# Performance work log

Hardware: AMD Instinct MI355X
Metric: run time of the kernel (lower is better)

Reference implementation:

```python
import jax, jax.numpy as jnp
from jax import lax
import numpy as np

BN_EPS = 1e-5

def nearest_resize(x, out_h, out_w):
    # torch F.interpolate(mode='nearest'): src = floor(dst * in / out)
    B, C, H, W = x.shape
    hi = (jnp.arange(out_h) * H) // out_h
    wi = (jnp.arange(out_w) * W) // out_w
    return x[:, :, hi][:, :, :, wi]

def conv1x1(x, w, b=None):
    y = jnp.einsum('bchw,oc->bohw', x, w)
    if b is not None:
        y = y + b[None, :, None, None]
    return y

def dwconv(x, w, stride, pad):
    C = x.shape[1]
    return lax.conv_general_dilated(x, w, (stride, stride), [(pad, pad), (pad, pad)],
                                    dimension_numbers=('NCHW', 'OIHW', 'NCHW'),
                                    feature_group_count=C)

def bn(x, g, b, m, v):
    scale = g / jnp.sqrt(v + BN_EPS)
    return (x - m[None, :, None, None]) * scale[None, :, None, None] + b[None, :, None, None]


def setup_inputs() -> dict:
    key = jax.random.key(0)
    ks = jax.random.split(key, 8)
    B, C, H0, W0 = 4, 512, 192, 192
    w_scale = 0.05
    return {
        'x': jax.random.normal(ks[0], (B, C, H0, W0), jnp.float32),
        'q_w': jax.random.normal(ks[1], (C, C), jnp.float32) * w_scale,
        'q_b': jnp.zeros((C,), jnp.float32),
        'kv_w': jax.random.normal(ks[2], (2 * C, C), jnp.float32) * w_scale,
        'kv_b': jnp.zeros((2 * C,), jnp.float32),
        'sr1_w': jax.random.normal(ks[3], (C, 1, 2, 2), jnp.float32) * w_scale,
        'bn1_g': jnp.ones((C,), jnp.float32),
        'bn1_b': jnp.zeros((C,), jnp.float32),
        'bn1_m': jnp.zeros((C,), jnp.float32),
        'bn1_v': jnp.ones((C,), jnp.float32),
        'sr2_w': jax.random.normal(ks[4], (C, C), jnp.float32) * w_scale,
        'bn2_g': jnp.ones((C,), jnp.float32),
        'bn2_b': jnp.zeros((C,), jnp.float32),
        'bn2_m': jnp.zeros((C,), jnp.float32),
        'bn2_v': jnp.ones((C,), jnp.float32),
        'lc_w': jax.random.normal(ks[5], (C, 1, 3, 3), jnp.float32) * w_scale,
        'lc_b': jnp.zeros((C,), jnp.float32),
        'head_num': 8,
    }


def reference(x, q_w, q_b, kv_w, kv_b, sr1_w, bn1_g, bn1_b, bn1_m, bn1_v,
              sr2_w, bn2_g, bn2_b, bn2_m, bn2_v, lc_w, lc_b, head_num):
    origin_h, origin_w = x.shape[2], x.shape[3]
    x = nearest_resize(x, origin_h // 4, origin_w // 4)
    B, C, H, W = x.shape
    hd = C // head_num
    scale = hd ** (-0.5)

    # q projection (1x1 conv with bias)
    q = conv1x1(x, q_w, q_b)  # [B,C,H,W]

    # spatial reduction: depthwise conv(k=sr, s=sr, p=sr//2) + BN + ReLU, then 1x1 + BN
    sr = sr1_w.shape[-1]
    kv = jax.nn.relu(bn(dwconv(x, sr1_w, sr, sr // 2), bn1_g, bn1_b, bn1_m, bn1_v))
    kv = bn(conv1x1(kv, sr2_w), bn2_g, bn2_b, bn2_m, bn2_v)

    # local depthwise 3x3 conv residual
    kv = dwconv(kv, lc_w, 1, 1) + lc_b[None, :, None, None] + kv

    # kv projection (1x1 conv, 2C output)
    kv = conv1x1(kv, kv_w, kv_b)
    k, v = jnp.split(kv, 2, axis=1)  # each [B,C,Hs,Ws]
    M = k.shape[2] * k.shape[3]

    q_ = jnp.swapaxes(q.reshape(B, head_num, hd, H * W), -1, -2)  # [B,h,N,hd]
    k_ = k.reshape(B, head_num, hd, M)                             # [B,h,hd,M]
    v_ = jnp.swapaxes(v.reshape(B, head_num, hd, M), -1, -2)       # [B,h,M,hd]

    attn = jax.nn.softmax(jnp.matmul(q_, k_) * scale, axis=-1)     # [B,h,N,M]
    out = jnp.swapaxes(jnp.matmul(attn, v_), -1, -2).reshape(B, C, H, W)

    # NOTE: original torch code passes size=(origin_w, origin_h)
    out = nearest_resize(out, origin_w, origin_h)
    return out
```

## Files before the change

kernel.cpp:

```cpp
#include <hip/hip_runtime.h>

#define Bsz 4
#define Cc  512
#define C2  1024
#define H0c 192
#define Hh  48
#define Nn  2304
#define HNh 8
#define HD  64
#define Hs  25
#define Ms  625

typedef const float* fp;
typedef _Float16 f16;
typedef __attribute__((ext_vector_type(8))) _Float16 f16x8;
typedef __attribute__((ext_vector_type(4))) _Float16 f16x4;
typedef __attribute__((ext_vector_type(4))) float    f32x4;

__global__ __launch_bounds__(256) void k_downsample(fp __restrict__ x,
                                                    float* __restrict__ xds) {
    int idx = blockIdx.x * 256 + threadIdx.x;
    if (idx >= Bsz * Cc * Nn) return;
    int j  = idx % Hh;
    int i  = (idx / Hh) % Hh;
    int bc = idx / Nn;
    xds[idx] = x[((size_t)bc * H0c + i * 4) * H0c + j * 4];
}

__global__ __launch_bounds__(256) void k_transpose(const float* __restrict__ in,
                                                   f16* __restrict__ out,
                                                   int R, int S,
                                                   size_t in_bs, size_t out_bs) {
    __shared__ float tile[32][33];
    const float* inb = in + (size_t)blockIdx.z * in_bs;
    f16* outb = out + (size_t)blockIdx.z * out_bs;
    int s0 = blockIdx.x * 32, r0 = blockIdx.y * 32;
    int t = threadIdx.x;
    #pragma unroll
    for (int p = 0; p < 4; p++) {
        int e = t + p * 256; int i = e >> 5, j = e & 31;
        float v = 0.f;
        if (r0 + i < R && s0 + j < S) v = inb[(size_t)(r0 + i) * S + s0 + j];
        tile[i][j] = v;
    }
    __syncthreads();
    #pragma unroll
    for (int p = 0; p < 4; p++) {
        int e = t + p * 256; int oi = e >> 5, oj = e & 31;
        if (s0 + oi < S && r0 + oj < R)
            outb[(size_t)(s0 + oi) * R + r0 + oj] = (f16)tile[oj][oi];
    }
}

__global__ __launch_bounds__(256) void k_gemm_mfma(
    const float* __restrict__ W, const f16* __restrict__ Xt,
    float* __restrict__ Yf, f16* __restrict__ Yt,
    const int Md, const int Nd, const int NtRows, const int mode,
    fp __restrict__ bias,
    fp __restrict__ bn_g, fp __restrict__ bn_b, fp __restrict__ bn_m, fp __restrict__ bn_v)
{
    __shared__ f16 sA[128 * 80];
    __shared__ f16 sB[128 * 80];
    const int b  = blockIdx.z;
    const int m0 = blockIdx.y * 128, n0 = blockIdx.x * 128;
    const int t = threadIdx.x;
    const int lane = t & 63, w = t >> 6;
    const int lm = lane & 15, q = lane >> 4;
    const int wm = w >> 1, wn = w & 1;
    const f16* Xb = Xt + (size_t)b * Nd * 512;

    f32x4 acc[4][4];
    #pragma unroll
    for (int i = 0; i < 4; i++)
        #pragma unroll
        for (int j = 0; j < 4; j++)
            #pragma unroll
            for (int r = 0; r < 4; r++) acc[i][j][r] = 0.f;

    for (int k0 = 0; k0 < 512; k0 += 64) {
        {
            int r = t >> 1, hh = (t & 1) * 32;
            const float* wr = W + (size_t)(m0 + r) * 512 + k0 + hh;
            f16* dst = &sA[r * 80 + hh];
            #pragma unroll
            for (int i = 0; i < 8; i++) {
                float4 v = *(const float4*)&wr[i * 4];
                f16x4 h4; h4[0] = (f16)v.x; h4[1] = (f16)v.y; h4[2] = (f16)v.z; h4[3] = (f16)v.w;
                *(f16x4*)&dst[i * 4] = h4;
            }
        }
        {
            int r = t >> 1, hh = (t & 1) * 32;
            bool ok = (n0 + r) < Nd;
            const f16* xr = Xb + (size_t)(n0 + r) * 512 + k0 + hh;
            f16* dst = &sB[r * 80 + hh];
            #pragma unroll
            for (int i = 0; i < 4; i++) {
                f16x8 v;
                if (ok) {
                    v = *(const f16x8*)&xr[i * 8];
                } else {
                    for (int z = 0; z < 8; z++) v[z] = (f16)0.f;
                }
                *(f16x8*)&dst[i * 8] = v;
            }
        }
        __syncthreads();
        #pragma unroll
        for (int ks = 0; ks < 2; ks++) {
            f16x8 af[4], bf[4];
            #pragma unroll
            for (int i = 0; i < 4; i++)
                af[i] = *(const f16x8*)&sA[(wm * 64 + i * 16 + lm) * 80 + ks * 32 + q * 8];
            #pragma unroll
            for (int j = 0; j < 4; j++)
                bf[j] = *(const f16x8*)&sB[(wn * 64 + j * 16 + lm) * 80 + ks * 32 + q * 8];
            #pragma unroll
            for (int i = 0; i < 4; i++)
                #pragma unroll
                for (int j = 0; j < 4; j++)
                    acc[i][j] = __builtin_amdgcn_mfma_f32_16x16x32_f16(af[i], bf[j], acc[i][j], 0, 0, 0);
        }
        __syncthreads();
    }

    #pragma unroll
    for (int i = 0; i < 4; i++) {
        int ob = m0 + wm * 64 + i * 16 + q * 4;
        float badd[4], bsc[4], bsh[4];
        #pragma unroll
        for (int r = 0; r < 4; r++) {
            int o = ob + r;
            badd[r] = bias ? bias[o] : 0.f;
            if (bn_g) { bsc[r] = bn_g[o] * rsqrtf(bn_v[o] + 1e-5f); bsh[r] = bn_b[o] - bn_m[o] * bsc[r]; }
            else      { bsc[r] = 1.f; bsh[r] = 0.f; }
        }
        #pragma unroll
        for (int j = 0; j < 4; j++) {
            int n = n0 + wn * 64 + j * 16 + lm;
            if (n >= Nd) continue;
            f32x4 a = acc[i][j];
            if (mode == 0) {
                #pragma unroll
                for (int r = 0; r < 4; r++)
                    Yf[((size_t)b * Md + ob + r) * Nd + n] = (a[r] + badd[r]) * bsc[r] + bsh[r];
            } else if (mode == 1 || (mode == 2 && ob < 512)) {
                f16x4 h;
                #pragma unroll
                for (int r = 0; r < 4; r++) h[r] = (f16)(a[r] + badd[r]);
                int hh = ob >> 6, d0 = ob & 63;
                *(f16x4*)&Yt[((size_t)(b * 8 + hh) * NtRows + n) * 64 + d0] = h;
            } else {
                #pragma unroll
                for (int r = 0; r < 4; r++)
                    Yf[((size_t)b * 512 + (ob + r - 512)) * Nd + n] = a[r] + badd[r];
            }
        }
    }
}

__global__ __launch_bounds__(256) void k_sr1(const float* __restrict__ xds, fp __restrict__ w,
                                             fp g, fp bb, fp bm, fp bv,
                                             float* __restrict__ kv1) {
    int idx = blockIdx.x * 256 + threadIdx.x;
    if (idx >= Bsz * Cc * Ms) return;
    int wo = idx % Hs, ho = (idx / Hs) % Hs, bc = idx / Ms;
    int c = bc % Cc;
    const float* src = xds + (size_t)bc * Nn;
    float acc = 0.f;
    #pragma unroll
    for (int di = 0; di < 2; di++) {
        int ih = ho * 2 - 1 + di;
        if (ih < 0 || ih >= Hh) continue;
        #pragma unroll
        for (int dj = 0; dj < 2; dj++) {
            int iw = wo * 2 - 1 + dj;
            if (iw < 0 || iw >= Hh) continue;
            acc += w[c * 4 + di * 2 + dj] * src[ih * Hh + iw];
        }
    }
    float sc = g[c] * rsqrtf(bv[c] + 1e-5f);
    float y = (acc - bm[c]) * sc + bb[c];
    kv1[idx] = fmaxf(y, 0.f);
}

__global__ __launch_bounds__(256) void k_lc(const float* __restrict__ kv2, fp __restrict__ w,
                                            fp __restrict__ lb, float* __restrict__ kv3) {
    int idx = blockIdx.x * 256 + threadIdx.x;
    if (idx >= Bsz * Cc * Ms) return;
    int wo = idx % Hs, ho = (idx / Hs) % Hs, bc = idx / Ms;
    int c = bc % Cc;
    const float* src = kv2 + (size_t)bc * Ms;
    float acc = 0.f;
    #pragma unroll
    for (int di = 0; di < 3; di++) {
        int ih = ho - 1 + di;
        if (ih < 0 || ih >= Hs) continue;
        #pragma unroll
        for (int dj = 0; dj < 3; dj++) {
            int iw = wo - 1 + dj;
            if (iw < 0 || iw >= Hs) continue;
            acc += w[c * 9 + di * 3 + dj] * src[ih * Hs + iw];
        }
    }
    kv3[idx] = acc + lb[c] + src[ho * Hs + wo];
}

__global__ __launch_bounds__(256) void k_cvtv(const float* __restrict__ vbuf,
                                              f16* __restrict__ vt) {
    int idx = blockIdx.x * 256 + threadIdx.x;
    if (idx >= Bsz * Cc * 640) return;
    int col = idx % 640, row = idx / 640;
    vt[idx] = (f16)((col < Ms) ? vbuf[(size_t)row * Ms + col] : 0.f);
}

__global__ __launch_bounds__(256) void k_attn_mfma(
    const f16* __restrict__ Qt, const f16* __restrict__ Kt,
    const f16* __restrict__ Vt, float* __restrict__ Obuf)
{
    __shared__ f16 sK[64 * 80];
    __shared__ f16 sV[64 * 80];
    __shared__ f16 sP[4][16 * 80];

    int bh = blockIdx.y;
    int n0 = blockIdx.x * 64;
    int t = threadIdx.x, w = t >> 6, lane = t & 63;
    int lm = lane & 15, q = lane >> 4;
    f16* sPw = &sP[w][0];

    f16x8 qf[2];
    {
        const f16* qrow = Qt + ((size_t)bh * Nn + n0 + w * 16 + lm) * 64;
        qf[0] = *(const f16x8*)&qrow[q * 8];
        qf[1] = *(const f16x8*)&qrow[32 + q * 8];
    }

    f32x4 od[4];
    #pragma unroll
    for (int dt = 0; dt < 4; dt++)
        #pragma unroll
        for (int r = 0; r < 4; r++) od[dt][r] = 0.f;
    float mold[4], lold[4];
    #pragma unroll
    for (int r = 0; r < 4; r++) { mold[r] = -1e30f; lold[r] = 0.f; }

    int kr = t >> 2, kc = t & 3;
    const f16* kbase = Kt + (size_t)bh * 640 * 64;
    const f16* vbase = Vt + (size_t)bh * 64 * 640;

    for (int mc = 0; mc < 640; mc += 64) {
        {
            const f16* ksrc = kbase + (size_t)(mc + kr) * 64;
            *(f16x8*)&sK[kr * 80 + kc * 8]      = *(const f16x8*)&ksrc[kc * 8];
            *(f16x8*)&sK[kr * 80 + 32 + kc * 8] = *(const f16x8*)&ksrc[32 + kc * 8];
            const f16* vsrc = vbase + (size_t)kr * 640 + mc;
            *(f16x8*)&sV[kr * 80 + kc * 8]      = *(const f16x8*)&vsrc[kc * 8];
            *(f16x8*)&sV[kr * 80 + 32 + kc * 8] = *(const f16x8*)&vsrc[32 + kc * 8];
        }
        __syncthreads();

        f32x4 sc4[4];
        #pragma unroll
        for (int j = 0; j < 4; j++)
            #pragma unroll
            for (int r = 0; r < 4; r++) sc4[j][r] = 0.f;
        #pragma unroll
        for (int ks = 0; ks < 2; ks++) {
            #pragma unroll
            for (int j = 0; j < 4; j++) {
                f16x8 kf = *(const f16x8*)&sK[(j * 16 + lm) * 80 + ks * 32 + q * 8];
                sc4[j] = __builtin_amdgcn_mfma_f32_16x16x32_f16(qf[ks], kf, sc4[j], 0, 0, 0);
            }
        }

        #pragma unroll
        for (int reg = 0; reg < 4; reg++) {
            float mx = -1e30f;
            #pragma unroll
            for (int j = 0; j < 4; j++) {
                float s = sc4[j][reg] * 0.125f;
                if (mc + j * 16 + lm >= Ms) s = -1e30f;
                sc4[j][reg] = s;
                mx = fmaxf(mx, s);
            }
            #pragma unroll
            for (int off = 1; off < 16; off <<= 1) mx = fmaxf(mx, __shfl_xor(mx, off));
            float mnew = fmaxf(mold[reg], mx);
            float alpha = __expf(mold[reg] - mnew);
            float rs = 0.f;
            #pragma unroll
            for (int j = 0; j < 4; j++) {
                float p = __expf(sc4[j][reg] - mnew);
                sc4[j][reg] = p;
                rs += p;
            }
            #pragma unroll
            for (int off = 1; off < 16; off <<= 1) rs += __shfl_xor(rs, off);
            lold[reg] = lold[reg] * alpha + rs;
            mold[reg] = mnew;
            #pragma unroll
            for (int dt = 0; dt < 4; dt++) od[dt][reg] *= alpha;
            #pragma unroll
            for (int j = 0; j < 4; j++)
                sPw[(q * 4 + reg) * 80 + j * 16 + lm] = (f16)sc4[j][reg];
        }

        #pragma unroll
        for (int ks = 0; ks < 2; ks++) {
            f16x8 pa = *(const f16x8*)&sPw[lm * 80 + ks * 32 + q * 8];
            #pragma unroll
            for (int dt = 0; dt < 4; dt++) {
                f16x8 vf = *(const f16x8*)&sV[(dt * 16 + lm) * 80 + ks * 32 + q * 8];
                od[dt] = __builtin_amdgcn_mfma_f32_16x16x32_f16(pa, vf, od[dt], 0, 0, 0);
            }
        }
        __syncthreads();
    }

    float inv[4];
    #pragma unroll
    for (int r = 0; r < 4; r++) inv[r] = 1.f / lold[r];
    #pragma unroll
    for (int dt = 0; dt < 4; dt++) {
        f32x4 o;
        #pragma unroll
        for (int r = 0; r < 4; r++) o[r] = od[dt][r] * inv[r];
        size_t c = (size_t)bh * 64 + dt * 16 + lm;
        *(f32x4*)&Obuf[c * Nn + n0 + w * 16 + q * 4] = o;
    }
}

__global__ __launch_bounds__(256) void k_upsample(const float* __restrict__ O,
                                                  float* __restrict__ out) {
    size_t idx = (size_t)blockIdx.x * 256 + threadIdx.x;
    if (idx >= (size_t)Bsz * Cc * H0c * 48) return;
    int jg = (int)(idx % 48);
    int i  = (int)((idx / 48) % H0c);
    int bc = (int)(idx / ((size_t)48 * H0c));
    float s = O[(size_t)bc * Nn + (i >> 2) * Hh + jg];
    float4 pack = make_float4(s, s, s, s);
    *(float4*)(out + ((size_t)bc * H0c + i) * H0c + jg * 4) = pack;
}

extern "C" void kernel_launch(void* const* d_in, const int* in_sizes, int n_in,
                              void* d_out, int out_size, void* d_ws, size_t ws_size,
                              hipStream_t stream) {
    (void)in_sizes; (void)n_in; (void)out_size; (void)ws_size;
    fp x     = (fp)d_in[0];
    fp q_w   = (fp)d_in[1];
    fp q_b   = (fp)d_in[2];
    fp kv_w  = (fp)d_in[3];
    fp kv_b  = (fp)d_in[4];
    fp sr1_w = (fp)d_in[5];
    fp bn1_g = (fp)d_in[6];
    fp bn1_b = (fp)d_in[7];
    fp bn1_m = (fp)d_in[8];
    fp bn1_v = (fp)d_in[9];
    fp sr2_w = (fp)d_in[10];
    fp bn2_g = (fp)d_in[11];
    fp bn2_b = (fp)d_in[12];
    fp bn2_m = (fp)d_in[13];
    fp bn2_v = (fp)d_in[14];
    fp lc_w  = (fp)d_in[15];
    fp lc_b  = (fp)d_in[16];
    float* out = (float*)d_out;

    float* ws   = (float*)d_ws;
    float* A    = ws;
    float* xds  = A;
    float* Obuf = A;
    float* kv3  = A + 3400000;
    float* Bv   = A + 4718592;
    f16*   xt   = (f16*)Bv;
    float* kv2  = Bv;
    float* Cq   = Bv + 2359296;
    f16*   Qt   = (f16*)Cq;
    float* Dv   = Cq + 2359296;
    float* kv1  = Dv;
    float* vbuf = Dv;
    float* Ev   = Dv + 1280000;
    f16*   kv1t = (f16*)Ev;
    f16*   kv3t = (f16*)Ev;
    float* Fv   = Ev + 640000;
    f16*   Kt   = (f16*)Fv;
    float* Gv   = Fv + 655360;
    f16*   vt   = (f16*)Gv;

    k_downsample<<<Bsz * Cc * Nn / 256, 256, 0, stream>>>(x, xds);
    k_transpose<<<dim3(72, 16, Bsz), 256, 0, stream>>>(xds, xt, Cc, Nn,
                                                       (size_t)Cc * Nn, (size_t)Nn * Cc);
    k_gemm_mfma<<<dim3(18, 4, Bsz), 256, 0, stream>>>(q_w, xt, nullptr, Qt,
        Cc, Nn, Nn, 1, q_b, nullptr, nullptr, nullptr, nullptr);
    k_sr1<<<Bsz * Cc * Ms / 256, 256, 0, stream>>>(xds, sr1_w, bn1_g, bn1_b, bn1_m, bn1_v, kv1);
    k_transpose<<<dim3(20, 16, Bsz), 256, 0, stream>>>(kv1, kv1t, Cc, Ms,
                                                       (size_t)Cc * Ms, (size_t)Ms * Cc);
    k_gemm_mfma<<<dim3(5, 4, Bsz), 256, 0, stream>>>(sr2_w, kv1t, kv2, nullptr,
        Cc, Ms, 0, 0, nullptr, bn2_g, bn2_b, bn2_m, bn2_v);
    k_lc<<<Bsz * Cc * Ms / 256, 256, 0, stream>>>(kv2, lc_w, lc_b, kv3);
    k_transpose<<<dim3(20, 16, Bsz), 256, 0, stream>>>(kv3, kv3t, Cc, Ms,
                                                       (size_t)Cc * Ms, (size_t)Ms * Cc);
    k_gemm_mfma<<<dim3(5, 8, Bsz), 256, 0, stream>>>(kv_w, kv3t, vbuf, Kt,
        C2, Ms, 640, 2, kv_b, nullptr, nullptr, nullptr, nullptr);
    k_cvtv<<<Bsz * Cc * 640 / 256, 256, 0, stream>>>(vbuf, vt);
    k_attn_mfma<<<dim3(Nn / 64, Bsz * HNh), 256, 0, stream>>>(Qt, Kt, vt, Obuf);
    k_upsample<<<(unsigned)((size_t)Bsz * Cc * H0c * 48 / 256), 256, 0, stream>>>(Obuf, out);
}
```

Baseline: 651.5 us.

## Fuse elementwise stages into neighbouring kernels and write upsampled output from attention

Merges the downsample with the transpose, the spatial-reduction depthwise conv and the local 3x3 conv with their transposes, and the V fp16 conversion into the kv GEMM epilogue. The attention kernel now writes the 4x4 nearest-upsampled output directly, which removes the Obuf round trip and the separate upsample launch. This cuts several kernel launches and intermediate fp32 buffers, and the workspace layout is reorganised to match. The attention epilogue's scattered float4 stores across rows may be less coalesced than the old dedicated upsample kernel.

```diff
diff --git a/kernel.cpp b/kernel.cpp
--- a/kernel.cpp
+++ b/kernel.cpp
@@ -17,44 +17,115 @@
 typedef __attribute__((ext_vector_type(4))) _Float16 f16x4;
 typedef __attribute__((ext_vector_type(4))) float    f32x4;
 
-__global__ __launch_bounds__(256) void k_downsample(fp __restrict__ x,
-                                                    float* __restrict__ xds) {
-    int idx = blockIdx.x * 256 + threadIdx.x;
-    if (idx >= Bsz * Cc * Nn) return;
-    int j  = idx % Hh;
-    int i  = (idx / Hh) % Hh;
-    int bc = idx / Nn;
-    xds[idx] = x[((size_t)bc * H0c + i * 4) * H0c + j * 4];
-}
-
-__global__ __launch_bounds__(256) void k_transpose(const float* __restrict__ in,
-                                                   f16* __restrict__ out,
-                                                   int R, int S,
-                                                   size_t in_bs, size_t out_bs) {
+__global__ __launch_bounds__(256) void k_ds_t(fp __restrict__ x,
+                                              float* __restrict__ xds,
+                                              f16* __restrict__ xt) {
     __shared__ float tile[32][33];
-    const float* inb = in + (size_t)blockIdx.z * in_bs;
-    f16* outb = out + (size_t)blockIdx.z * out_bs;
-    int s0 = blockIdx.x * 32, r0 = blockIdx.y * 32;
-    int t = threadIdx.x;
+    const int b = blockIdx.z;
+    const int s0 = blockIdx.x * 32, r0 = blockIdx.y * 32;
+    const int t = threadIdx.x;
+    const float* xb = x + (size_t)b * Cc * H0c * H0c;
+    float* xdsb = xds + (size_t)b * Cc * Nn;
     #pragma unroll
     for (int p = 0; p < 4; p++) {
         int e = t + p * 256; int i = e >> 5, j = e & 31;
+        int c = r0 + i, n = s0 + j;
+        float v = xb[((size_t)c * H0c + (n / Hh) * 4) * H0c + (n % Hh) * 4];
+        tile[i][j] = v;
+        xdsb[(size_t)c * Nn + n] = v;
+    }
+    __syncthreads();
+    #pragma unroll
+    for (int p = 0; p < 4; p++) {
+        int e = t + p * 256; int oi = e >> 5, oj = e & 31;
+        xt[((size_t)b * Nn + s0 + oi) * Cc + r0 + oj] = (f16)tile[oj][oi];
+    }
+}
+
+__global__ __launch_bounds__(256) void k_sr1t(const float* __restrict__ xds,
+                                              fp __restrict__ w, fp g, fp bb, fp bm, fp bv,
+                                              f16* __restrict__ kv1t) {
+    __shared__ float tile[32][33];
+    const int b = blockIdx.z;
+    const int s0 = blockIdx.x * 32, r0 = blockIdx.y * 32;
+    const int t = threadIdx.x;
+    #pragma unroll
+    for (int p = 0; p < 4; p++) {
+        int e = t + p * 256; int i = e >> 5, j = e & 31;
+        int c = r0 + i, n = s0 + j;
         float v = 0.f;
-        if (r0 + i < R && s0 + j < S) v = inb[(size_t)(r0 + i) * S + s0 + j];
+        if (n < Ms) {
+            int ho = n / Hs, wo = n % Hs;
+            const float* src = xds + ((size_t)b * Cc + c) * Nn;
+            float acc = 0.f;
+            #pragma unroll
+            for (int di = 0; di < 2; di++) {
+                int ih = ho * 2 - 1 + di;
+                if (ih < 0 || ih >= Hh) continue;
+                #pragma unroll
+                for (int dj = 0; dj < 2; dj++) {
+                    int iw = wo * 2 - 1 + dj;
+                    if (iw < 0 || iw >= Hh) continue;
+                    acc += w[c * 4 + di * 2 + dj] * src[ih * Hh + iw];
+                }
+            }
+            float sc = g[c] * rsqrtf(bv[c] + 1e-5f);
+            v = fmaxf((acc - bm[c]) * sc + bb[c], 0.f);
+        }
         tile[i][j] = v;
     }
     __syncthreads();
     #pragma unroll
     for (int p = 0; p < 4; p++) {
         int e = t + p * 256; int oi = e >> 5, oj = e & 31;
-        if (s0 + oi < S && r0 + oj < R)
-            outb[(size_t)(s0 + oi) * R + r0 + oj] = (f16)tile[oj][oi];
+        if (s0 + oi < Ms)
+            kv1t[((size_t)b * Ms + s0 + oi) * Cc + r0 + oj] = (f16)tile[oj][oi];
+    }
+}
+
+__global__ __launch_bounds__(256) void k_lct(const float* __restrict__ kv2,
+                                             fp __restrict__ w, fp __restrict__ lb,
+                                             f16* __restrict__ kv3t) {
+    __shared__ float tile[32][33];
+    const int b = blockIdx.z;
+    const int s0 = blockIdx.x * 32, r0 = blockIdx.y * 32;
+    const int t = threadIdx.x;
+    #pragma unroll
+    for (int p = 0; p < 4; p++) {
+        int e = t + p * 256; int i = e >> 5, j = e & 31;
+        int c = r0 + i, n = s0 + j;
+        float v = 0.f;
+        if (n < Ms) {
+            int ho = n / Hs, wo = n % Hs;
+            const float* src = kv2 + ((size_t)b * Cc + c) * Ms;
+            float acc = 0.f;
+            #pragma unroll
+            for (int di = 0; di < 3; di++) {
+                int ih = ho - 1 + di;
+                if (ih < 0 || ih >= Hs) continue;
+                #pragma unroll
+                for (int dj = 0; dj < 3; dj++) {
+                    int iw = wo - 1 + dj;
+                    if (iw < 0 || iw >= Hs) continue;
+                    acc += w[c * 9 + di * 3 + dj] * src[ih * Hs + iw];
+                }
+            }
+            v = acc + lb[c] + src[n];
+        }
+        tile[i][j] = v;
+    }
+    __syncthreads();
+    #pragma unroll
+    for (int p = 0; p < 4; p++) {
+        int e = t + p * 256; int oi = e >> 5, oj = e & 31;
+        if (s0 + oi < Ms)
+            kv3t[((size_t)b * Ms + s0 + oi) * Cc + r0 + oj] = (f16)tile[oj][oi];
     }
 }
 
 __global__ __launch_bounds__(256) void k_gemm_mfma(
     const float* __restrict__ W, const f16* __restrict__ Xt,
-    float* __restrict__ Yf, f16* __restrict__ Yt,
+    float* __restrict__ Yf, f16* __restrict__ Yt, f16* __restrict__ Vt,
     const int Md, const int Nd, const int NtRows, const int mode,
     fp __restrict__ bias,
     fp __restrict__ bn_g, fp __restrict__ bn_b, fp __restrict__ bn_m, fp __restrict__ bn_v)
@@ -138,12 +209,13 @@
         #pragma unroll
         for (int j = 0; j < 4; j++) {
             int n = n0 + wn * 64 + j * 16 + lm;
-            if (n >= Nd) continue;
             f32x4 a = acc[i][j];
             if (mode == 0) {
-                #pragma unroll
-                for (int r = 0; r < 4; r++)
-                    Yf[((size_t)b * Md + ob + r) * Nd + n] = (a[r] + badd[r]) * bsc[r] + bsh[r];
+                if (n < Nd) {
+                    #pragma unroll
+                    for (int r = 0; r < 4; r++)
+                        Yf[((size_t)b * Md + ob + r) * Nd + n] = (a[r] + badd[r]) * bsc[r] + bsh[r];
+                }
             } else if (mode == 1 || (mode == 2 && ob < 512)) {
                 f16x4 h;
                 #pragma unroll
@@ -152,71 +224,18 @@
                 *(f16x4*)&Yt[((size_t)(b * 8 + hh) * NtRows + n) * 64 + d0] = h;
             } else {
                 #pragma unroll
-                for (int r = 0; r < 4; r++)
-                    Yf[((size_t)b * 512 + (ob + r - 512)) * Nd + n] = a[r] + badd[r];
-            }
-        }
-    }
-}
-
-__global__ __launch_bounds__(256) void k_sr1(const float* __restrict__ xds, fp __restrict__ w,
-                                             fp g, fp bb, fp bm, fp bv,
-                                             float* __restrict__ kv1) {
-    int idx = blockIdx.x * 256 + threadIdx.x;
-    if (idx >= Bsz * Cc * Ms) return;
-    int wo = idx % Hs, ho = (idx / Hs) % Hs, bc = idx / Ms;
-    int c = bc % Cc;
-    const float* src = xds + (size_t)bc * Nn;
-    float acc = 0.f;
-    #pragma unroll
-    for (int di = 0; di < 2; di++) {
-        int ih = ho * 2 - 1 + di;
-        if (ih < 0 || ih >= Hh) continue;
-        #pragma unroll
-        for (int dj = 0; dj < 2; dj++) {
-            int iw = wo * 2 - 1 + dj;
-            if (iw < 0 || iw >= Hh) continue;
-            acc += w[c * 4 + di * 2 + dj] * src[ih * Hh + iw];
-        }
-    }
-    float sc = g[c] * rsqrtf(bv[c] + 1e-5f);
-    float y = (acc - bm[c]) * sc + bb[c];
-    kv1[idx] = fmaxf(y, 0.f);
-}
-
-__global__ __launch_bounds__(256) void k_lc(const float* __restrict__ kv2, fp __restrict__ w,
-                                            fp __restrict__ lb, float* __restrict__ kv3) {
-    int idx = blockIdx.x * 256 + threadIdx.x;
-    if (idx >= Bsz * Cc * Ms) return;
-    int wo = idx % Hs, ho = (idx / Hs) % Hs, bc = idx / Ms;
-    int c = bc % Cc;
-    const float* src = kv2 + (size_t)bc * Ms;
-    float acc = 0.f;
-    #pragma unroll
-    for (int di = 0; di < 3; di++) {
-        int ih = ho - 1 + di;
-        if (ih < 0 || ih >= Hs) continue;
-        #pragma unroll
-        for (int dj = 0; dj < 3; dj++) {
-            int iw = wo - 1 + dj;
-            if (iw < 0 || iw >= Hs) continue;
-            acc += w[c * 9 + di * 3 + dj] * src[ih * Hs + iw];
-        }
-    }
-    kv3[idx] = acc + lb[c] + src[ho * Hs + wo];
-}
-
-__global__ __launch_bounds__(256) void k_cvtv(const float* __restrict__ vbuf,
-                                              f16* __restrict__ vt) {
-    int idx = blockIdx.x * 256 + threadIdx.x;
-    if (idx >= Bsz * Cc * 640) return;
-    int col = idx % 640, row = idx / 640;
-    vt[idx] = (f16)((col < Ms) ? vbuf[(size_t)row * Ms + col] : 0.f);
+                for (int r = 0; r < 4; r++) {
+                    float val = (n < Nd) ? (a[r] + badd[r]) : 0.f;
+                    Vt[((size_t)b * Cc + (ob + r - 512)) * 640 + n] = (f16)val;
+                }
+            }
+        }
+    }
 }
 
 __global__ __launch_bounds__(256) void k_attn_mfma(
     const f16* __restrict__ Qt, const f16* __restrict__ Kt,
-    const f16* __restrict__ Vt, float* __restrict__ Obuf)
+    const f16* __restrict__ Vt, float* __restrict__ out)
 {
     __shared__ f16 sK[64 * 80];
     __shared__ f16 sV[64 * 80];
@@ -317,29 +336,24 @@
         __syncthreads();
     }
 
-    float inv[4];
-    #pragma unroll
-    for (int r = 0; r < 4; r++) inv[r] = 1.f / lold[r];
+    float inv4[4];
+    #pragma unroll
+    for (int r = 0; r < 4; r++) inv4[r] = 1.f / lold[r];
+    const int bq = bh >> 3, hch = (bh & 7) * 64;
+    const int nq = n0 + w * 16 + q * 4;
+    const int i4 = (nq / Hh) * 4, j4 = (nq % Hh) * 4;
     #pragma unroll
     for (int dt = 0; dt < 4; dt++) {
-        f32x4 o;
-        #pragma unroll
-        for (int r = 0; r < 4; r++) o[r] = od[dt][r] * inv[r];
-        size_t c = (size_t)bh * 64 + dt * 16 + lm;
-        *(f32x4*)&Obuf[c * Nn + n0 + w * 16 + q * 4] = o;
-    }
-}
-
-__global__ __launch_bounds__(256) void k_upsample(const float* __restrict__ O,
-                                                  float* __restrict__ out) {
-    size_t idx = (size_t)blockIdx.x * 256 + threadIdx.x;
-    if (idx >= (size_t)Bsz * Cc * H0c * 48) return;
-    int jg = (int)(idx % 48);
-    int i  = (int)((idx / 48) % H0c);
-    int bc = (int)(idx / ((size_t)48 * H0c));
-    float s = O[(size_t)bc * Nn + (i >> 2) * Hh + jg];
-    float4 pack = make_float4(s, s, s, s);
-    *(float4*)(out + ((size_t)bc * H0c + i) * H0c + jg * 4) = pack;
+        float* oc = out + ((size_t)(bq * Cc + hch + dt * 16 + lm) * H0c + i4) * H0c + j4;
+        #pragma unroll
+        for (int r = 0; r < 4; r++) {
+            float val = od[dt][r] * inv4[r];
+            float4 pk = make_float4(val, val, val, val);
+            #pragma unroll
+            for (int ii = 0; ii < 4; ii++)
+                *(float4*)&oc[ii * H0c + r * 4] = pk;
+        }
+    }
 }
 
 extern "C" void kernel_launch(void* const* d_in, const int* in_sizes, int n_in,
@@ -366,42 +380,23 @@
     float* out = (float*)d_out;
 
     float* ws   = (float*)d_ws;
-    float* A    = ws;
-    float* xds  = A;
-    float* Obuf = A;
-    float* kv3  = A + 3400000;
-    float* Bv   = A + 4718592;
-    f16*   xt   = (f16*)Bv;
-    float* kv2  = Bv;
-    float* Cq   = Bv + 2359296;
-    f16*   Qt   = (f16*)Cq;
-    float* Dv   = Cq + 2359296;
-    float* kv1  = Dv;
-    float* vbuf = Dv;
-    float* Ev   = Dv + 1280000;
-    f16*   kv1t = (f16*)Ev;
-    f16*   kv3t = (f16*)Ev;
-    float* Fv   = Ev + 640000;
-    f16*   Kt   = (f16*)Fv;
-    float* Gv   = Fv + 655360;
-    f16*   vt   = (f16*)Gv;
-
-    k_downsample<<<Bsz * Cc * Nn / 256, 256, 0, stream>>>(x, xds);
-    k_transpose<<<dim3(72, 16, Bsz), 256, 0, stream>>>(xds, xt, Cc, Nn,
-                                                       (size_t)Cc * Nn, (size_t)Nn * Cc);
-    k_gemm_mfma<<<dim3(18, 4, Bsz), 256, 0, stream>>>(q_w, xt, nullptr, Qt,
+    float* xds  = ws;
+    float* kv2  = ws;
+    f16*   Kt   = (f16*)(ws + 1310720);
+    f16*   vt   = (f16*)(ws + 1966080);
+    f16*   xt   = (f16*)(ws + 4718592);
+    f16*   kv1t = (f16*)(ws + 4718592);
+    f16*   kv3t = (f16*)(ws + 5358592);
+    f16*   Qt   = (f16*)(ws + 7077888);
+
+    k_ds_t<<<dim3(72, 16, Bsz), 256, 0, stream>>>(x, xds, xt);
+    k_gemm_mfma<<<dim3(18, 4, Bsz), 256, 0, stream>>>(q_w, xt, nullptr, Qt, nullptr,
         Cc, Nn, Nn, 1, q_b, nullptr, nullptr, nullptr, nullptr);
-    k_sr1<<<Bsz * Cc * Ms / 256, 256, 0, stream>>>(xds, sr1_w, bn1_g, bn1_b, bn1_m, bn1_v, kv1);
-    k_transpose<<<dim3(20, 16, Bsz), 256, 0, stream>>>(kv1, kv1t, Cc, Ms,
-                                                       (size_t)Cc * Ms, (size_t)Ms * Cc);
-    k_gemm_mfma<<<dim3(5, 4, Bsz), 256, 0, stream>>>(sr2_w, kv1t, kv2, nullptr,
+    k_sr1t<<<dim3(20, 16, Bsz), 256, 0, stream>>>(xds, sr1_w, bn1_g, bn1_b, bn1_m, bn1_v, kv1t);
+    k_gemm_mfma<<<dim3(5, 4, Bsz), 256, 0, stream>>>(sr2_w, kv1t, kv2, nullptr, nullptr,
         Cc, Ms, 0, 0, nullptr, bn2_g, bn2_b, bn2_m, bn2_v);
-    k_lc<<<Bsz * Cc * Ms / 256, 256, 0, stream>>>(kv2, lc_w, lc_b, kv3);
-    k_transpose<<<dim3(20, 16, Bsz), 256, 0, stream>>>(kv3, kv3t, Cc, Ms,
-                                                       (size_t)Cc * Ms, (size_t)Ms * Cc);
-    k_gemm_mfma<<<dim3(5, 8, Bsz), 256, 0, stream>>>(kv_w, kv3t, vbuf, Kt,
+    k_lct<<<dim3(20, 16, Bsz), 256, 0, stream>>>(kv2, lc_w, lc_b, kv3t);
+    k_gemm_mfma<<<dim3(5, 8, Bsz), 256, 0, stream>>>(kv_w, kv3t, nullptr, Kt, vt,
         C2, Ms, 640, 2, kv_b, nullptr, nullptr, nullptr, nullptr);
-    k_cvtv<<<Bsz * Cc * 640 / 256, 256, 0, stream>>>(vbuf, vt);
-    k_attn_mfma<<<dim3(Nn / 64, Bsz * HNh), 256, 0, stream>>>(Qt, Kt, vt, Obuf);
-    k_upsample<<<(unsigned)((size_t)Bsz * Cc * H0c * 48 / 256), 256, 0, stream>>>(Obuf, out);
-}
+    k_attn_mfma<<<dim3(Nn / 64, Bsz * HNh), 256, 0, stream>>>(Qt, Kt, vt, out);
+}
```

Result: slower. 690.5 us (+6.0%).
